# Performance work log

Measured on AMD Instinct MI355X. Metric: run time of the kernel, lower is better.

The kernel has to match this reference:

```python
import jax, jax.numpy as jnp
import numpy as np

NEG_SLOPE = 0.01  # torch LeakyReLU default
HID = 20
NLAYERS = 50
DIN = 3
DOUT = 3

def leaky(z):
    return jnp.where(z >= 0, z, NEG_SLOPE * z)

def setup_inputs() -> dict:
    key = jax.random.key(0)
    ks = jax.random.split(key, 10)
    B = 2_000_000
    x = jax.random.normal(ks[0], (B, DIN), dtype=jnp.float32)
    s_in = 1.0 / np.sqrt(DIN)
    s_h = 1.0 / np.sqrt(HID)
    lift_w = jax.random.uniform(ks[1], (DIN, HID), jnp.float32, -s_in, s_in)
    lift_b = jax.random.uniform(ks[2], (HID,), jnp.float32, -s_in, s_in)
    W1 = jax.random.uniform(ks[3], (NLAYERS, HID, HID), jnp.float32, -s_h, s_h)
    b1 = jax.random.uniform(ks[4], (NLAYERS, HID), jnp.float32, -s_h, s_h)
    W2 = jax.random.uniform(ks[5], (NLAYERS, HID, HID), jnp.float32, -s_h, s_h)
    b2 = jax.random.uniform(ks[6], (NLAYERS, HID), jnp.float32, -s_h, s_h)
    dts = jax.random.normal(ks[7], (NLAYERS,), dtype=jnp.float32)
    proj_w = jax.random.uniform(ks[8], (HID, DOUT), jnp.float32, -s_h, s_h)
    proj_b = jax.random.uniform(ks[9], (DOUT,), jnp.float32, -s_h, s_h)
    return {"x": x, "lift_w": lift_w, "lift_b": lift_b, "W1": W1, "b1": b1,
            "W2": W2, "b2": b2, "dts": dts, "proj_w": proj_w, "proj_b": proj_b}

def reference(x, lift_w, lift_b, W1, b1, W2, b2, dts, proj_w, proj_b):
    # lift: [B, DIN] -> [B, HID]
    h = x @ lift_w + lift_b

    def step(h, layer):
        w1, bb1, w2, bb2, dt = layer
        h = h + dt * leaky(leaky(h @ w1 + bb1) @ w2 + bb2)
        return h, None

    h, _ = jax.lax.scan(step, h, (W1, b1, W2, b2, dts))
    return h @ proj_w + proj_b
```

## Files before the change

### kernel.cpp

```cpp
#include <hip/hip_runtime.h>


#define HID 20
#define NLAYERS 50
#define NEG 0.01f

typedef _Float16 half8   __attribute__((ext_vector_type(8)));
typedef _Float16 half2v  __attribute__((ext_vector_type(2)));
typedef __fp16   fp16x2  __attribute__((ext_vector_type(2)));
typedef float    floatx16 __attribute__((ext_vector_type(16)));
typedef unsigned uint4v  __attribute__((ext_vector_type(4)));

__device__ __forceinline__ unsigned pack_rne(float a, float b) {
    half2v p;
    p[0] = (_Float16)a;
    p[1] = (_Float16)b;
    return __builtin_bit_cast(unsigned, p);
}

__device__ __forceinline__ int phi(int k) {
    if (k >= 4 && k < 8)  return k + 4;
    if (k >= 8 && k < 12) return k - 4;
    return k;
}

__global__ void build_wfrags(const float* __restrict__ W1, const float* __restrict__ b1,
                             const float* __restrict__ W2, const float* __restrict__ b2,
                             const float* __restrict__ dts,
                             half8* __restrict__ wf)
{
    const int L = blockIdx.x;
    const int l = threadIdx.x;
    const int m = l & 31, hh = l >> 5;
    const float* Ws[2] = { W1 + L * HID * HID, W2 + L * HID * HID };
    const float* bs[2] = { b1 + L * HID,       b2 + L * HID };
#pragma unroll
    for (int mk = 0; mk < 2; ++mk) {
#pragma unroll
        for (int ks = 0; ks < 2; ++ks) {
            half8 frag;
#pragma unroll
            for (int j = 0; j < 8; ++j) {
                int k = ks * 16 + hh * 8 + j;
                float v = 0.0f;
                if (m < HID) {
                    if (k < HID) v = Ws[mk][phi(k) * HID + m];
                    else if (k == HID) v = bs[mk][m];
                }
                frag[j] = (_Float16)v;
            }
            wf[((L * 2 + mk) * 2 + ks) * 64 + l] = frag;
        }
    }
    if (l == 0) {
        unsigned* dtp = (unsigned*)(wf + NLAYERS * 256);
        const __fp16 d = (__fp16)dts[L];
        fp16x2 dp = {d, d};
        dtp[L] = __builtin_bit_cast(unsigned, dp);
    }
}

__global__ __launch_bounds__(256, 4) void unet_mfma(
    const float* __restrict__ x,
    const float* __restrict__ lift_w,
    const float* __restrict__ lift_b,
    const float* __restrict__ proj_w,
    const float* __restrict__ proj_b,
    const half8* __restrict__ wf,
    float* __restrict__ out, int Bn)
{
    const int tid = threadIdx.x;
    const int wv  = tid >> 6;
    const int l   = tid & 63;
    const int n   = l & 31;
    const int hh  = l >> 5;

    const int g  = blockIdx.x * 128 + wv * 32 + n;
    const int gi = g < Bn ? g : Bn - 1;

    const float x0 = x[3 * gi + 0];
    const float x1 = x[3 * gi + 1];
    const float x2 = x[3 * gi + 2];

    unsigned hp[6];
#pragma unroll
    for (int i = 0; i < 6; ++i) {
        const int r0   = 2 * i;
        const int row0 = (r0 & 3) + 8 * (r0 >> 2) + 4 * hh;
        float v[2];
#pragma unroll
        for (int e = 0; e < 2; ++e) {
            const int row = row0 + e;
            if (row < HID) {
                float a = lift_b[row];
                a = fmaf(x0, lift_w[0 * HID + row], a);
                a = fmaf(x1, lift_w[1 * HID + row], a);
                a = fmaf(x2, lift_w[2 * HID + row], a);
                v[e] = a;
            } else {
                v[e] = 0.0f;
            }
        }
        hp[i] = pack_rne(v[0], v[1]);
    }
    fp16x2 h[6];
#pragma unroll
    for (int i = 0; i < 6; ++i) h[i] = __builtin_bit_cast(fp16x2, hp[i]);

    const unsigned C10 = 0x00003C00u;
    const fp16x2  negs = {(__fp16)NEG, (__fp16)NEG};

    floatx16 zf;
#pragma unroll
    for (int i = 0; i < 16; ++i) zf[i] = 0.0f;

    const unsigned* __restrict__ dtp = (const unsigned*)(wf + NLAYERS * 256);
    const half8* __restrict__ wp = wf + l;

    half8 bh0 = __builtin_bit_cast(half8, (uint4v){hp[0], hp[1], hp[2], hp[3]});
    half8 bh1 = __builtin_bit_cast(half8, (uint4v){hp[4], hp[5], C10, 0u});

    for (int L = 0; L < NLAYERS; ++L) {
        const half8 a10 = wp[0];
        const half8 a11 = wp[64];
        const half8 a20 = wp[128];
        const half8 a21 = wp[192];
        wp += 256;
        const fp16x2 dt2 = __builtin_bit_cast(fp16x2, dtp[L]);

        floatx16 acc = __builtin_amdgcn_mfma_f32_32x32x16_f16(a10, bh0, zf, 0, 0, 0);
        acc = __builtin_amdgcn_mfma_f32_32x32x16_f16(a11, bh1, acc, 0, 0, 0);

        unsigned tp[6];
#pragma unroll
        for (int i = 0; i < 6; ++i) {
            fp16x2 z  = __builtin_amdgcn_cvt_pkrtz(acc[2 * i], acc[2 * i + 1]);
            fp16x2 t2 = __builtin_elementwise_max(z, z * negs);
            tp[i] = __builtin_bit_cast(unsigned, t2);
        }
        const half8 bt0 = __builtin_bit_cast(half8, (uint4v){tp[0], tp[1], tp[2], tp[3]});
        const half8 bt1 = __builtin_bit_cast(half8, (uint4v){tp[4], tp[5], C10, 0u});

        floatx16 acc2 = __builtin_amdgcn_mfma_f32_32x32x16_f16(a20, bt0, zf, 0, 0, 0);
        acc2 = __builtin_amdgcn_mfma_f32_32x32x16_f16(a21, bt1, acc2, 0, 0, 0);

#pragma unroll
        for (int i = 0; i < 6; ++i) {
            fp16x2 z  = __builtin_amdgcn_cvt_pkrtz(acc2[2 * i], acc2[2 * i + 1]);
            fp16x2 lz = __builtin_elementwise_max(z, z * negs);
            h[i] = __builtin_elementwise_fma(dt2, lz, h[i]);
            hp[i] = __builtin_bit_cast(unsigned, h[i]);
        }
        bh0 = __builtin_bit_cast(half8, (uint4v){hp[0], hp[1], hp[2], hp[3]});
        bh1 = __builtin_bit_cast(half8, (uint4v){hp[4], hp[5], C10, 0u});
    }

    float po0 = 0.f, po1 = 0.f, po2 = 0.f;
#pragma unroll
    for (int i = 0; i < 6; ++i) {
#pragma unroll
        for (int e = 0; e < 2; ++e) {
            const int r0  = 2 * i;
            const int row = (r0 & 3) + 8 * (r0 >> 2) + 4 * hh + e;
            const float hv = (row < HID) ? (float)h[i][e] : 0.0f;
            const int rowc = (row < HID) ? row : 0;
            po0 = fmaf(hv, proj_w[rowc * 3 + 0], po0);
            po1 = fmaf(hv, proj_w[rowc * 3 + 1], po1);
            po2 = fmaf(hv, proj_w[rowc * 3 + 2], po2);
        }
    }
    po0 += __shfl_xor(po0, 32, 64);
    po1 += __shfl_xor(po1, 32, 64);
    po2 += __shfl_xor(po2, 32, 64);
    if (hh == 0 && g < Bn) {
        out[3 * g + 0] = po0 + proj_b[0];
        out[3 * g + 1] = po1 + proj_b[1];
        out[3 * g + 2] = po2 + proj_b[2];
    }
}

extern "C" void kernel_launch(void* const* d_in, const int* in_sizes, int n_in,
                              void* d_out, int out_size, void* d_ws, size_t ws_size,
                              hipStream_t stream) {
    const float* x      = (const float*)d_in[0];
    const float* lift_w = (const float*)d_in[1];
    const float* lift_b = (const float*)d_in[2];
    const float* W1     = (const float*)d_in[3];
    const float* b1     = (const float*)d_in[4];
    const float* W2     = (const float*)d_in[5];
    const float* b2     = (const float*)d_in[6];
    const float* dts    = (const float*)d_in[7];
    const float* proj_w = (const float*)d_in[8];
    const float* proj_b = (const float*)d_in[9];
    float* out = (float*)d_out;

    const int B = in_sizes[0] / 3;
    half8* wf = (half8*)d_ws;

    build_wfrags<<<NLAYERS, 64, 0, stream>>>(W1, b1, W2, b2, dts, wf);

    const int blocks = (B + 127) / 128;
    unet_mfma<<<blocks, 256, 0, stream>>>(
        x, lift_w, lift_b, proj_w, proj_b, wf, out, B);
}
```

Measured before the change: 571.1 us.

## Process two 32-sample tiles per wave and prefetch next layer weights

```diff
diff --git a/kernel.cpp b/kernel.cpp
--- a/kernel.cpp
+++ b/kernel.cpp
@@ -75,107 +75,146 @@
     const int n   = l & 31;
     const int hh  = l >> 5;
 
-    const int g  = blockIdx.x * 128 + wv * 32 + n;
-    const int gi = g < Bn ? g : Bn - 1;
-
-    const float x0 = x[3 * gi + 0];
-    const float x1 = x[3 * gi + 1];
-    const float x2 = x[3 * gi + 2];
-
-    unsigned hp[6];
-#pragma unroll
-    for (int i = 0; i < 6; ++i) {
-        const int r0   = 2 * i;
-        const int row0 = (r0 & 3) + 8 * (r0 >> 2) + 4 * hh;
-        float v[2];
-#pragma unroll
-        for (int e = 0; e < 2; ++e) {
-            const int row = row0 + e;
-            if (row < HID) {
-                float a = lift_b[row];
-                a = fmaf(x0, lift_w[0 * HID + row], a);
-                a = fmaf(x1, lift_w[1 * HID + row], a);
-                a = fmaf(x2, lift_w[2 * HID + row], a);
-                v[e] = a;
-            } else {
-                v[e] = 0.0f;
-            }
-        }
-        hp[i] = pack_rne(v[0], v[1]);
-    }
-    fp16x2 h[6];
-#pragma unroll
-    for (int i = 0; i < 6; ++i) h[i] = __builtin_bit_cast(fp16x2, hp[i]);
+    const int gA  = blockIdx.x * 256 + wv * 64 + n;
+    const int gB  = gA + 32;
+    const int giA = gA < Bn ? gA : Bn - 1;
+    const int giB = gB < Bn ? gB : Bn - 1;
 
     const unsigned C10 = 0x00003C00u;
     const fp16x2  negs = {(__fp16)NEG, (__fp16)NEG};
 
+    fp16x2 hA[6], hB[6];
+    unsigned hpA[6], hpB[6];
+    {
+        const float xA0 = x[3 * giA + 0], xA1 = x[3 * giA + 1], xA2 = x[3 * giA + 2];
+        const float xB0 = x[3 * giB + 0], xB1 = x[3 * giB + 1], xB2 = x[3 * giB + 2];
+#pragma unroll
+        for (int i = 0; i < 6; ++i) {
+            const int r0   = 2 * i;
+            const int row0 = (r0 & 3) + 8 * (r0 >> 2) + 4 * hh;
+            float vA[2], vB[2];
+#pragma unroll
+            for (int e = 0; e < 2; ++e) {
+                const int row = row0 + e;
+                if (row < HID) {
+                    const float w0 = lift_w[0 * HID + row];
+                    const float w1 = lift_w[1 * HID + row];
+                    const float w2 = lift_w[2 * HID + row];
+                    const float b  = lift_b[row];
+                    vA[e] = fmaf(xA2, w2, fmaf(xA1, w1, fmaf(xA0, w0, b)));
+                    vB[e] = fmaf(xB2, w2, fmaf(xB1, w1, fmaf(xB0, w0, b)));
+                } else { vA[e] = 0.0f; vB[e] = 0.0f; }
+            }
+            hpA[i] = pack_rne(vA[0], vA[1]);
+            hpB[i] = pack_rne(vB[0], vB[1]);
+        }
+    }
+#pragma unroll
+    for (int i = 0; i < 6; ++i) {
+        hA[i] = __builtin_bit_cast(fp16x2, hpA[i]);
+        hB[i] = __builtin_bit_cast(fp16x2, hpB[i]);
+    }
+
     floatx16 zf;
 #pragma unroll
     for (int i = 0; i < 16; ++i) zf[i] = 0.0f;
 
     const unsigned* __restrict__ dtp = (const unsigned*)(wf + NLAYERS * 256);
-    const half8* __restrict__ wp = wf + l;
-
-    half8 bh0 = __builtin_bit_cast(half8, (uint4v){hp[0], hp[1], hp[2], hp[3]});
-    half8 bh1 = __builtin_bit_cast(half8, (uint4v){hp[4], hp[5], C10, 0u});
+
+    half8 bhA0 = __builtin_bit_cast(half8, (uint4v){hpA[0], hpA[1], hpA[2], hpA[3]});
+    half8 bhA1 = __builtin_bit_cast(half8, (uint4v){hpA[4], hpA[5], C10, 0u});
+    half8 bhB0 = __builtin_bit_cast(half8, (uint4v){hpB[0], hpB[1], hpB[2], hpB[3]});
+    half8 bhB1 = __builtin_bit_cast(half8, (uint4v){hpB[4], hpB[5], C10, 0u});
+
+    const half8* __restrict__ wl = wf + l;
+    half8 c0 = wl[0], c1 = wl[64], c2 = wl[128], c3 = wl[192];
 
     for (int L = 0; L < NLAYERS; ++L) {
-        const half8 a10 = wp[0];
-        const half8 a11 = wp[64];
-        const half8 a20 = wp[128];
-        const half8 a21 = wp[192];
-        wp += 256;
+        const int Ln = (L + 1 < NLAYERS) ? (L + 1) : (NLAYERS - 1);
+        const half8* __restrict__ wn = wf + l + Ln * 256;
+        const half8 p0 = wn[0], p1 = wn[64], p2 = wn[128], p3 = wn[192];
+
         const fp16x2 dt2 = __builtin_bit_cast(fp16x2, dtp[L]);
 
-        floatx16 acc = __builtin_amdgcn_mfma_f32_32x32x16_f16(a10, bh0, zf, 0, 0, 0);
-        acc = __builtin_amdgcn_mfma_f32_32x32x16_f16(a11, bh1, acc, 0, 0, 0);
-
-        unsigned tp[6];
+        floatx16 accA = __builtin_amdgcn_mfma_f32_32x32x16_f16(c0, bhA0, zf, 0, 0, 0);
+        floatx16 accB = __builtin_amdgcn_mfma_f32_32x32x16_f16(c0, bhB0, zf, 0, 0, 0);
+        accA = __builtin_amdgcn_mfma_f32_32x32x16_f16(c1, bhA1, accA, 0, 0, 0);
+        accB = __builtin_amdgcn_mfma_f32_32x32x16_f16(c1, bhB1, accB, 0, 0, 0);
+
+        unsigned tpA[6], tpB[6];
 #pragma unroll
         for (int i = 0; i < 6; ++i) {
-            fp16x2 z  = __builtin_amdgcn_cvt_pkrtz(acc[2 * i], acc[2 * i + 1]);
-            fp16x2 t2 = __builtin_elementwise_max(z, z * negs);
-            tp[i] = __builtin_bit_cast(unsigned, t2);
-        }
-        const half8 bt0 = __builtin_bit_cast(half8, (uint4v){tp[0], tp[1], tp[2], tp[3]});
-        const half8 bt1 = __builtin_bit_cast(half8, (uint4v){tp[4], tp[5], C10, 0u});
-
-        floatx16 acc2 = __builtin_amdgcn_mfma_f32_32x32x16_f16(a20, bt0, zf, 0, 0, 0);
-        acc2 = __builtin_amdgcn_mfma_f32_32x32x16_f16(a21, bt1, acc2, 0, 0, 0);
+            fp16x2 zA = __builtin_amdgcn_cvt_pkrtz(accA[2 * i], accA[2 * i + 1]);
+            fp16x2 zB = __builtin_amdgcn_cvt_pkrtz(accB[2 * i], accB[2 * i + 1]);
+            fp16x2 tA = __builtin_elementwise_max(zA, zA * negs);
+            fp16x2 tB = __builtin_elementwise_max(zB, zB * negs);
+            tpA[i] = __builtin_bit_cast(unsigned, tA);
+            tpB[i] = __builtin_bit_cast(unsigned, tB);
+        }
+        const half8 btA0 = __builtin_bit_cast(half8, (uint4v){tpA[0], tpA[1], tpA[2], tpA[3]});
+        const half8 btA1 = __builtin_bit_cast(half8, (uint4v){tpA[4], tpA[5], C10, 0u});
+        const half8 btB0 = __builtin_bit_cast(half8, (uint4v){tpB[0], tpB[1], tpB[2], tpB[3]});
+        const half8 btB1 = __builtin_bit_cast(half8, (uint4v){tpB[4], tpB[5], C10, 0u});
+
+        floatx16 acc2A = __builtin_amdgcn_mfma_f32_32x32x16_f16(c2, btA0, zf, 0, 0, 0);
+        floatx16 acc2B = __builtin_amdgcn_mfma_f32_32x32x16_f16(c2, btB0, zf, 0, 0, 0);
+        acc2A = __builtin_amdgcn_mfma_f32_32x32x16_f16(c3, btA1, acc2A, 0, 0, 0);
+        acc2B = __builtin_amdgcn_mfma_f32_32x32x16_f16(c3, btB1, acc2B, 0, 0, 0);
 
 #pragma unroll
         for (int i = 0; i < 6; ++i) {
-            fp16x2 z  = __builtin_amdgcn_cvt_pkrtz(acc2[2 * i], acc2[2 * i + 1]);
-            fp16x2 lz = __builtin_elementwise_max(z, z * negs);
-            h[i] = __builtin_elementwise_fma(dt2, lz, h[i]);
-            hp[i] = __builtin_bit_cast(unsigned, h[i]);
-        }
-        bh0 = __builtin_bit_cast(half8, (uint4v){hp[0], hp[1], hp[2], hp[3]});
-        bh1 = __builtin_bit_cast(half8, (uint4v){hp[4], hp[5], C10, 0u});
-    }
-
-    float po0 = 0.f, po1 = 0.f, po2 = 0.f;
+            fp16x2 zA = __builtin_amdgcn_cvt_pkrtz(acc2A[2 * i], acc2A[2 * i + 1]);
+            fp16x2 zB = __builtin_amdgcn_cvt_pkrtz(acc2B[2 * i], acc2B[2 * i + 1]);
+            fp16x2 lA = __builtin_elementwise_max(zA, zA * negs);
+            fp16x2 lB = __builtin_elementwise_max(zB, zB * negs);
+            hA[i] = __builtin_elementwise_fma(dt2, lA, hA[i]);
+            hB[i] = __builtin_elementwise_fma(dt2, lB, hB[i]);
+            hpA[i] = __builtin_bit_cast(unsigned, hA[i]);
+            hpB[i] = __builtin_bit_cast(unsigned, hB[i]);
+        }
+        bhA0 = __builtin_bit_cast(half8, (uint4v){hpA[0], hpA[1], hpA[2], hpA[3]});
+        bhA1 = __builtin_bit_cast(half8, (uint4v){hpA[4], hpA[5], C10, 0u});
+        bhB0 = __builtin_bit_cast(half8, (uint4v){hpB[0], hpB[1], hpB[2], hpB[3]});
+        bhB1 = __builtin_bit_cast(half8, (uint4v){hpB[4], hpB[5], C10, 0u});
+
+        c0 = p0; c1 = p1; c2 = p2; c3 = p3;
+    }
+
+    float aO0 = 0.f, aO1 = 0.f, aO2 = 0.f, bO0 = 0.f, bO1 = 0.f, bO2 = 0.f;
 #pragma unroll
     for (int i = 0; i < 6; ++i) {
 #pragma unroll
         for (int e = 0; e < 2; ++e) {
             const int r0  = 2 * i;
             const int row = (r0 & 3) + 8 * (r0 >> 2) + 4 * hh + e;
-            const float hv = (row < HID) ? (float)h[i][e] : 0.0f;
-            const int rowc = (row < HID) ? row : 0;
-            po0 = fmaf(hv, proj_w[rowc * 3 + 0], po0);
-            po1 = fmaf(hv, proj_w[rowc * 3 + 1], po1);
-            po2 = fmaf(hv, proj_w[rowc * 3 + 2], po2);
-        }
-    }
-    po0 += __shfl_xor(po0, 32, 64);
-    po1 += __shfl_xor(po1, 32, 64);
-    po2 += __shfl_xor(po2, 32, 64);
-    if (hh == 0 && g < Bn) {
-        out[3 * g + 0] = po0 + proj_b[0];
-        out[3 * g + 1] = po1 + proj_b[1];
-        out[3 * g + 2] = po2 + proj_b[2];
+            if (row < HID) {
+                const float w0 = proj_w[row * 3 + 0];
+                const float w1 = proj_w[row * 3 + 1];
+                const float w2 = proj_w[row * 3 + 2];
+                const float va = (float)hA[i][e];
+                const float vb = (float)hB[i][e];
+                aO0 = fmaf(va, w0, aO0); aO1 = fmaf(va, w1, aO1); aO2 = fmaf(va, w2, aO2);
+                bO0 = fmaf(vb, w0, bO0); bO1 = fmaf(vb, w1, bO1); bO2 = fmaf(vb, w2, bO2);
+            }
+        }
+    }
+    aO0 += __shfl_xor(aO0, 32, 64);
+    aO1 += __shfl_xor(aO1, 32, 64);
+    aO2 += __shfl_xor(aO2, 32, 64);
+    bO0 += __shfl_xor(bO0, 32, 64);
+    bO1 += __shfl_xor(bO1, 32, 64);
+    bO2 += __shfl_xor(bO2, 32, 64);
+    if (hh == 0) {
+        if (gA < Bn) {
+            out[3 * gA + 0] = aO0 + proj_b[0];
+            out[3 * gA + 1] = aO1 + proj_b[1];
+            out[3 * gA + 2] = aO2 + proj_b[2];
+        }
+        if (gB < Bn) {
+            out[3 * gB + 0] = bO0 + proj_b[0];
+            out[3 * gB + 1] = bO1 + proj_b[1];
+            out[3 * gB + 2] = bO2 + proj_b[2];
+        }
     }
 }
 
@@ -199,7 +238,7 @@
 
     build_wfrags<<<NLAYERS, 64, 0, stream>>>(W1, b1, W2, b2, dts, wf);
 
-    const int blocks = (B + 127) / 128;
+    const int blocks = (B + 255) / 256;
     unet_mfma<<<blocks, 256, 0, stream>>>(
         x, lift_w, lift_b, proj_w, proj_b, wf, out, B);
 }
```

Result: faster. 474.9 us (-16.8%).
